# Performance work log

Hardware: AMD Instinct MI355X
Metric: run time of the kernel (lower is better)

The kernel has to match this reference:

```python
import jax, jax.numpy as jnp
import numpy as np
from jax import lax

HIDDEN = 64
EPS = 1e-6


def setup_inputs() -> dict:
    key = jax.random.key(0)
    ks = jax.random.split(key, 7)
    B, S, H = 2048, 2048, HIDDEN
    scale_ih = 1.0 / np.sqrt(2.0)
    scale_hh = 1.0 / np.sqrt(H)
    return {
        "residuals": jax.random.normal(ks[0], (B, S), dtype=jnp.float32),
        "W_ih_w": jax.random.uniform(ks[1], (H, 2), jnp.float32, -scale_ih, scale_ih),
        "W_ih_b": jax.random.uniform(ks[2], (H,), jnp.float32, -scale_ih, scale_ih),
        "W_hh_w": jax.random.uniform(ks[3], (H, H), jnp.float32, -scale_hh, scale_hh),
        "W_hh_b": jax.random.uniform(ks[4], (H,), jnp.float32, -scale_hh, scale_hh),
        "fc_w": jax.random.uniform(ks[5], (1, H), jnp.float32, -scale_hh, scale_hh),
        "fc_b": jax.random.uniform(ks[6], (1,), jnp.float32, -scale_hh, scale_hh),
    }


def reference(residuals, W_ih_w, W_ih_b, W_hh_w, W_hh_b, fc_w, fc_b):
    B, S = residuals.shape
    H = W_hh_w.shape[0]
    # torch.var is unbiased (ddof=1)
    sigma0 = jnp.var(residuals, axis=1, ddof=1)  # (B,)
    h0 = jnp.zeros((B, H), dtype=residuals.dtype)

    def step(carry, eps_prev):
        h, sigma = carry  # (B,H), (B,)
        inp = jnp.stack([eps_prev * eps_prev, sigma], axis=1)  # (B,2)
        h = inp @ W_ih_w.T + W_ih_b + h @ W_hh_w.T + W_hh_b  # (B,H)
        sigma = jax.nn.softplus(h @ fc_w.T + fc_b)[:, 0] + EPS  # (B,)
        return (h, sigma), sigma

    # eps at steps t=1..S-1 uses residuals[:, t-1]
    (_, _), sigmas = lax.scan(step, (h0, sigma0), residuals[:, :-1].T)  # (S-1, B)
    cond_vars = jnp.concatenate([sigma0[:, None], sigmas.T], axis=1)  # (B, S)
    return cond_vars
```

## Files before the change

kernel.cpp:

```cpp
#include <hip/hip_runtime.h>

#define S_LEN 2048

typedef float f32x4 __attribute__((ext_vector_type(4)));

__device__ __forceinline__ float rlane(float v, int l) {
    return __int_as_float(__builtin_amdgcn_readlane(__float_as_int(v), l));
}

template<int CTRL, int RM>
__device__ __forceinline__ float dpp_add(float v) {
    int t = __builtin_amdgcn_update_dpp(0, __float_as_int(v), CTRL, RM, 0xF, true);
    return v + __int_as_float(t);
}
__device__ __forceinline__ float wave_sum(float v) {
    v = dpp_add<0x111, 0xF>(v);
    v = dpp_add<0x112, 0xF>(v);
    v = dpp_add<0x114, 0xF>(v);
    v = dpp_add<0x118, 0xF>(v);
    v = dpp_add<0x142, 0xA>(v);
    v = dpp_add<0x143, 0xC>(v);
    return rlane(v, 63);
}
__device__ __forceinline__ float half_sum(float v, bool hf) {
    v = dpp_add<0x111, 0xF>(v);
    v = dpp_add<0x112, 0xF>(v);
    v = dpp_add<0x114, 0xF>(v);
    v = dpp_add<0x118, 0xF>(v);
    v = dpp_add<0x142, 0xA>(v);
    const float lo = rlane(v, 31);
    const float hi = rlane(v, 63);
    return hf ? hi : lo;
}

#if __has_builtin(__builtin_amdgcn_exp2f)
#define EXP2F(x) __builtin_amdgcn_exp2f(x)
#else
#define EXP2F(x) exp2f(x)
#endif
#if __has_builtin(__builtin_amdgcn_logf)
#define LOG2F(x) __builtin_amdgcn_logf(x)
#else
#define LOG2F(x) __log2f(x)
#endif

__attribute__((amdgpu_flat_work_group_size(512, 512)))
__attribute__((amdgpu_waves_per_eu(4, 8)))
__global__ void garch_fused(
    const float* __restrict__ res,
    const float* __restrict__ Wih,
    const float* __restrict__ bih,
    const float* __restrict__ Whh,
    const float* __restrict__ bhh,
    const float* __restrict__ fcw,
    const float* __restrict__ fcb,
    float* __restrict__ out)
{
    __shared__ __align__(16) float Wl[4096];
    __shared__ __align__(16) float tabA[1024];
    __shared__ __align__(16) float tabB[1024];
    __shared__ __align__(16) float ring[1024];
    __shared__ __align__(16) float ubuf[64];
    __shared__ float alpS[32], betS[32], gpreS[32], scS[4];

    const int tid  = threadIdx.x;
    const int lane = tid & 63;
    const int wv   = tid >> 6;
    const int l    = lane & 31;
    const bool hf  = (lane >= 32);

    const float Kc  = 1.44269504088896340736f;
    const float LN2 = 0.69314718055994530942f;

    {
        const f32x4* w4 = (const f32x4*)Whh;
        f32x4* wl4 = (f32x4*)Wl;
        for (int i = tid; i < 1024; i += 512) wl4[i] = w4[i];
    }
    __syncthreads();

    const int rp = blockIdx.x;
    const int p  = wv;
    const float* __restrict__ row  = res + (size_t)(2 * rp + (hf ? 1 : 0)) * S_LEN;
    float* __restrict__       orow = out + (size_t)(2 * rp + (hf ? 1 : 0)) * S_LEN;

    float* __restrict__ ringw = &ring[wv * 128 + (hf ? 64 : 0)];
    const int rotaddr = ((lane & 32) | ((l + 31) & 31)) << 2;

    float varh = 0.f, sigK = 0.f, carry = 0.f, ldn, eN_hold;
    int c0w, warm;

    if (p == 0) {
        float s1 = 0.f, s2 = 0.f;
#pragma unroll 8
        for (int i = 0; i < 64; ++i) {
            const float x = row[i * 32 + l];
            s1 += x;
            s2 = fmaf(x, x, s2);
        }
        s1 = half_sum(s1, hf);
        s2 = half_sum(s2, hf);
        const float mean = s1 * (1.0f / S_LEN);
        varh = (s2 - s1 * mean) * (1.0f / (S_LEN - 1));
        sigK = Kc * varh;
        carry = sigK;

        const float e0 = row[l], e1 = row[32 + l];
        ringw[l] = e0 * e0;
        ringw[32 + l] = 0.f;
        eN_hold = e1 * e1;
        ldn = row[64 + l];
        c0w = 0; warm = 0;
    } else {
        const int cw0 = 8 * p - 1;
        const float eP = row[(cw0 - 1) * 32 + l];
        const float eC = row[cw0 * 32 + l];
        const float eN = row[(cw0 + 1) * 32 + l];
        ringw[((cw0 - 1) & 1) * 32 + l] = eP * eP;
        ringw[(cw0 & 1) * 32 + l]       = eC * eC;
        eN_hold = eN * eN;
        ldn = row[(cw0 + 2) * 32 + l];
        c0w = cw0; warm = 1;
    }
    asm volatile("" ::: "memory");

    if (wv == 7) {
        const float w0l = Wih[lane * 2], w1l = Wih[lane * 2 + 1];
        const float blp = bih[lane] + bhh[lane];
        const float fl  = fcw[lane];

        const float A0  = Kc * wave_sum(fl * w0l);
        const float b0t = wave_sum(fl * w1l);
        const float Cg  = Kc * (wave_sum(fl * blp) + fcb[0]);
        if (lane == 0) { alpS[0] = A0; betS[0] = b0t; }
        float gpre_ = Cg, ginf_ = Cg;

        ubuf[lane] = fl;
        asm volatile("" ::: "memory");
        const f32x4* uq4 = (const f32x4*)ubuf;
        float u;
        {
            float n0 = 0.f, n1 = 0.f, n2 = 0.f, n3 = 0.f;
#pragma unroll 4
            for (int q = 0; q < 16; ++q) {
                const f32x4 uq = uq4[q];
                n0 = fmaf(Wl[(4 * q + 0) * 64 + lane], uq.x, n0);
                n1 = fmaf(Wl[(4 * q + 1) * 64 + lane], uq.y, n1);
                n2 = fmaf(Wl[(4 * q + 2) * 64 + lane], uq.z, n2);
                n3 = fmaf(Wl[(4 * q + 3) * 64 + lane], uq.w, n3);
            }
            u = (n0 + n1) + (n2 + n3);
        }
#pragma unroll 1
        for (int i = 1; i < 48; ++i) {
            const float daK = Kc * wave_sum(u * w0l);
            const float dbT = wave_sum(u * w1l);
            const float dgK = Kc * wave_sum(u * blp);
            if (lane == 0 && i < 32) { alpS[i] = daK; betS[i] = dbT; }
            gpre_ += (lane >= i) ? dgK : 0.f;
            ginf_ += dgK;
            ubuf[lane] = u;
            asm volatile("" ::: "memory");
            float n0 = 0.f, n1 = 0.f, n2 = 0.f, n3 = 0.f;
#pragma unroll 4
            for (int q = 0; q < 16; ++q) {
                const f32x4 uq = uq4[q];
                n0 = fmaf(Wl[(4 * q + 0) * 64 + lane], uq.x, n0);
                n1 = fmaf(Wl[(4 * q + 1) * 64 + lane], uq.y, n1);
                n2 = fmaf(Wl[(4 * q + 2) * 64 + lane], uq.z, n2);
                n3 = fmaf(Wl[(4 * q + 3) * 64 + lane], uq.w, n3);
            }
            u = (n0 + n1) + (n2 + n3);
        }
        asm volatile("" ::: "memory");
        for (int f = lane; f < 1024; f += 64) {
            const int lr = f >> 5, jc = f & 31;
            const int m = (lr - jc) & 31;
            const int dst = (((jc >> 2) * 32 + lr) << 2) + (jc & 3);
            tabA[dst] = (m < 4) ? 0.f : alpS[m];
            tabB[dst] = (m < 4) ? 0.f : betS[m];
        }
        if (lane < 32) gpreS[lane] = gpre_;
        if (lane == 0) scS[0] = ginf_;
    }
    __syncthreads();

    const float ginf = scS[0];
    const float bb0 = betS[0], bb1 = betS[1], bb2 = betS[2], bb3 = betS[3];
    const float Ka0 = alpS[0], Ka1 = alpS[1], Ka2 = alpS[2], Ka3 = alpS[3];

#define FIR4(DST, SB) { \
    const int a0_ = ((SB) << 5) + l; \
    const float x0_ = ringw[a0_]; \
    const float x1_ = ringw[(a0_ - 1) & 63]; \
    const float x2_ = ringw[(a0_ - 2) & 63]; \
    const float x3_ = ringw[(a0_ - 3) & 63]; \
    (DST) = fmaf(Ka3, x3_, fmaf(Ka2, x2_, fmaf(Ka1, x1_, Ka0 * x0_))); }

#define BCASTI(DST, V, IDX) { \
    const float lo_ = rlane((V), (IDX)); \
    const float hi_ = rlane((V), 32 + (IDX)); \
    (DST) = hf ? hi_ : lo_; }

    const f32x4* tA4 = (const f32x4*)tabA;
    const f32x4* tB4 = (const f32x4*)tabB;

    float acc, p1, p2, p3, vout = 0.f;

    if (p == 0) {
        float e4C;
        FIR4(e4C, 0);
        acc = gpreS[l] + e4C;
        BCASTI(p1, acc, 0); BCASTI(p2, acc, 1); BCASTI(p3, acc, 2);
        ringw[32 + l] = eN_hold;
        asm volatile("" ::: "memory");
    } else {
        const int cw0 = 8 * p - 1;
        float e4C;
        FIR4(e4C, cw0 & 1);
        acc = ginf + e4C;
        const f32x4* pq = (const f32x4*)(ringw + ((cw0 - 1) & 1) * 32);
#pragma unroll
        for (int q = 0; q < 8; ++q) {
            const f32x4 aqv = tA4[q * 32 + l];
            const f32x4 eq = pq[q];
#pragma unroll
            for (int w = 0; w < 4; ++w) {
                const int j = 4 * q + w;
                const float cf = (j > l) ? aqv[w] : 0.f;
                acc = fmaf(cf, eq[w], acc);
            }
        }
        BCASTI(p1, acc, 0); BCASTI(p2, acc, 1); BCASTI(p3, acc, 2);
        sigK = 0.f; carry = 0.f;
        ringw[((cw0 + 1) & 1) * 32 + l] = eN_hold;
        asm volatile("" ::: "memory");
    }

    const int ncc = 8 + warm;
    const bool p0 = (p == 0);

#pragma unroll 1
    for (int cc = 0; cc < ncc; ++cc) {
        const int c = c0w + cc;
        const int s = c & 1;
        float e4N;
        FIR4(e4N, s ^ 1);
        const float ginfE = ginf + e4N;
        const float sigchunk = carry;
        const f32x4* ringq = (const f32x4*)(ringw + (s << 5));

#pragma unroll
        for (int jg = 0; jg < 4; ++jg) {
            const f32x4 caq0 = tA4[(2 * jg) * 32 + l];
            const f32x4 caq1 = tA4[(2 * jg + 1) * 32 + l];
            const f32x4 cbq0 = tB4[(2 * jg) * 32 + l];
            const f32x4 cbq1 = tB4[(2 * jg + 1) * 32 + l];
            const f32x4 curA = ringq[jg * 2];
            const f32x4 curB = ringq[jg * 2 + 1];
#pragma unroll
            for (int k = 0; k < 8; ++k) {
                const int jj = (jg << 3) + k;
                const float ash = (k < 4) ? caq0[k] : caq1[k - 4];
                const float bsh = (k < 4) ? cbq0[k] : cbq1[k - 4];
                const float e2j = (k < 4) ? curA[k] : curB[k - 4];
                const float xp = fmaf(bb0, sigK, p1);
                acc = fmaf(bsh, sigK, acc);
                acc = fmaf(ash, e2j, acc);
                const bool mine = (l == jj);
                acc = mine ? ginfE : acc;
                const float tlo = rlane(acc, (jj + 3) & 31);
                const float thi = rlane(acc, 32 + ((jj + 3) & 31));
                const float t = hf ? thi : tlo;
                p1 = fmaf(bb1, sigK, p2);
                p2 = fmaf(bb2, sigK, p3);
                p3 = fmaf(bb3, sigK, t);
                const float ee = EXP2F(-__builtin_fabsf(xp));
                sigK = fmaxf(xp, 0.f) + LOG2F(1.0f + ee);
                vout = mine ? sigK : vout;
            }
        }

        if (cc >= warm) {
            const float rotv = __int_as_float(
                __builtin_amdgcn_ds_bpermute(rotaddr, __float_as_int(vout)));
            const float sv = (l == 0) ? sigchunk : rotv;
            float outv = fmaf(sv, LN2, 1e-6f);
            if (p0 && cc == 0) outv = (l == 0) ? varh : outv;
            orow[(c << 5) + l] = outv;
        }
        {
            const float c1v = rlane(vout, 31);
            const float c2v = rlane(vout, 63);
            carry = hf ? c2v : c1v;
        }
        ringw[(s << 5) + l] = ldn * ldn;
        const int nc3 = (c + 3 < 63) ? (c + 3) : 63;
        ldn = row[nc3 * 32 + l];
        asm volatile("" ::: "memory");
    }
#undef FIR4
#undef BCASTI
}

extern "C" void kernel_launch(void* const* d_in, const int* in_sizes, int n_in,
                              void* d_out, int out_size, void* d_ws, size_t ws_size,
                              hipStream_t stream) {
    const float* res = (const float*)d_in[0];
    const float* Wih = (const float*)d_in[1];
    const float* bih = (const float*)d_in[2];
    const float* Whh = (const float*)d_in[3];
    const float* bhh = (const float*)d_in[4];
    const float* fcw = (const float*)d_in[5];
    const float* fcb = (const float*)d_in[6];
    float* out = (float*)d_out;

    hipLaunchKernelGGL(garch_fused, dim3(1024), dim3(512), 0, stream,
                       res, Wih, bih, Whh, bhh, fcw, fcb, out);
}
```

Measured before the change: 213.7 us.

## Halve waves per row-pair and keep FIR coefficient tables in registers

Each block now uses 4 waves instead of 8, so each wave processes 16 chunks of 32 steps rather than 8. This halves the redundant warm-up and recompute work across the time-parallel waves. The per-lane alpha/beta coefficient tables move from LDS (tabA/tabB) into 64 VGPRs per lane, which removes LDS loads from the serial inner loop. The costs are a longer serial chain per wave and higher register pressure, which may reduce occupancy.

```diff
diff --git a/kernel.cpp b/kernel.cpp
--- a/kernel.cpp
+++ b/kernel.cpp
@@ -44,7 +44,7 @@
 #define LOG2F(x) __log2f(x)
 #endif
 
-__attribute__((amdgpu_flat_work_group_size(512, 512)))
+__attribute__((amdgpu_flat_work_group_size(256, 256)))
 __attribute__((amdgpu_waves_per_eu(4, 8)))
 __global__ void garch_fused(
     const float* __restrict__ res,
@@ -57,9 +57,7 @@
     float* __restrict__ out)
 {
     __shared__ __align__(16) float Wl[4096];
-    __shared__ __align__(16) float tabA[1024];
-    __shared__ __align__(16) float tabB[1024];
-    __shared__ __align__(16) float ring[1024];
+    __shared__ __align__(16) float ring[512];
     __shared__ __align__(16) float ubuf[64];
     __shared__ float alpS[32], betS[32], gpreS[32], scS[4];
 
@@ -75,7 +73,7 @@
     {
         const f32x4* w4 = (const f32x4*)Whh;
         f32x4* wl4 = (f32x4*)Wl;
-        for (int i = tid; i < 1024; i += 512) wl4[i] = w4[i];
+        for (int i = tid; i < 1024; i += 256) wl4[i] = w4[i];
     }
     __syncthreads();
 
@@ -112,7 +110,7 @@
         ldn = row[64 + l];
         c0w = 0; warm = 0;
     } else {
-        const int cw0 = 8 * p - 1;
+        const int cw0 = 16 * p - 1;
         const float eP = row[(cw0 - 1) * 32 + l];
         const float eC = row[cw0 * 32 + l];
         const float eN = row[(cw0 + 1) * 32 + l];
@@ -124,7 +122,7 @@
     }
     asm volatile("" ::: "memory");
 
-    if (wv == 7) {
+    if (wv == 3) {
         const float w0l = Wih[lane * 2], w1l = Wih[lane * 2 + 1];
         const float blp = bih[lane] + bhh[lane];
         const float fl  = fcw[lane];
@@ -173,13 +171,6 @@
             u = (n0 + n1) + (n2 + n3);
         }
         asm volatile("" ::: "memory");
-        for (int f = lane; f < 1024; f += 64) {
-            const int lr = f >> 5, jc = f & 31;
-            const int m = (lr - jc) & 31;
-            const int dst = (((jc >> 2) * 32 + lr) << 2) + (jc & 3);
-            tabA[dst] = (m < 4) ? 0.f : alpS[m];
-            tabB[dst] = (m < 4) ? 0.f : betS[m];
-        }
         if (lane < 32) gpreS[lane] = gpre_;
         if (lane == 0) scS[0] = ginf_;
     }
@@ -188,6 +179,22 @@
     const float ginf = scS[0];
     const float bb0 = betS[0], bb1 = betS[1], bb2 = betS[2], bb3 = betS[3];
     const float Ka0 = alpS[0], Ka1 = alpS[1], Ka2 = alpS[2], Ka3 = alpS[3];
+
+    f32x4 ca[8], cb[8];
+#pragma unroll
+    for (int q = 0; q < 8; ++q) {
+#pragma unroll
+        for (int w = 0; w < 4; ++w) {
+            const int m = (l - (4 * q + w)) & 31;
+            const bool z = (m < 4);
+            ca[q][w] = z ? 0.f : alpS[m];
+            cb[q][w] = z ? 0.f : betS[m];
+        }
+    }
+    asm("" : "+v"(ca[0]), "+v"(ca[1]), "+v"(ca[2]), "+v"(ca[3]),
+             "+v"(ca[4]), "+v"(ca[5]), "+v"(ca[6]), "+v"(ca[7]),
+             "+v"(cb[0]), "+v"(cb[1]), "+v"(cb[2]), "+v"(cb[3]),
+             "+v"(cb[4]), "+v"(cb[5]), "+v"(cb[6]), "+v"(cb[7]));
 
 #define FIR4(DST, SB) { \
     const int a0_ = ((SB) << 5) + l; \
@@ -202,9 +209,6 @@
     const float hi_ = rlane((V), 32 + (IDX)); \
     (DST) = hf ? hi_ : lo_; }
 
-    const f32x4* tA4 = (const f32x4*)tabA;
-    const f32x4* tB4 = (const f32x4*)tabB;
-
     float acc, p1, p2, p3, vout = 0.f;
 
     if (p == 0) {
@@ -215,19 +219,18 @@
         ringw[32 + l] = eN_hold;
         asm volatile("" ::: "memory");
     } else {
-        const int cw0 = 8 * p - 1;
+        const int cw0 = 16 * p - 1;
         float e4C;
         FIR4(e4C, cw0 & 1);
         acc = ginf + e4C;
         const f32x4* pq = (const f32x4*)(ringw + ((cw0 - 1) & 1) * 32);
 #pragma unroll
         for (int q = 0; q < 8; ++q) {
-            const f32x4 aqv = tA4[q * 32 + l];
             const f32x4 eq = pq[q];
 #pragma unroll
             for (int w = 0; w < 4; ++w) {
                 const int j = 4 * q + w;
-                const float cf = (j > l) ? aqv[w] : 0.f;
+                const float cf = (j > l) ? ca[q][w] : 0.f;
                 acc = fmaf(cf, eq[w], acc);
             }
         }
@@ -237,7 +240,7 @@
         asm volatile("" ::: "memory");
     }
 
-    const int ncc = 8 + warm;
+    const int ncc = 16 + warm;
     const bool p0 = (p == 0);
 
 #pragma unroll 1
@@ -252,17 +255,13 @@
 
 #pragma unroll
         for (int jg = 0; jg < 4; ++jg) {
-            const f32x4 caq0 = tA4[(2 * jg) * 32 + l];
-            const f32x4 caq1 = tA4[(2 * jg + 1) * 32 + l];
-            const f32x4 cbq0 = tB4[(2 * jg) * 32 + l];
-            const f32x4 cbq1 = tB4[(2 * jg + 1) * 32 + l];
             const f32x4 curA = ringq[jg * 2];
             const f32x4 curB = ringq[jg * 2 + 1];
 #pragma unroll
             for (int k = 0; k < 8; ++k) {
                 const int jj = (jg << 3) + k;
-                const float ash = (k < 4) ? caq0[k] : caq1[k - 4];
-                const float bsh = (k < 4) ? cbq0[k] : cbq1[k - 4];
+                const float ash = ca[jj >> 2][jj & 3];
+                const float bsh = cb[jj >> 2][jj & 3];
                 const float e2j = (k < 4) ? curA[k] : curB[k - 4];
                 const float xp = fmaf(bb0, sigK, p1);
                 acc = fmaf(bsh, sigK, acc);
@@ -315,6 +314,6 @@
     const float* fcb = (const float*)d_in[6];
     float* out = (float*)d_out;
 
-    hipLaunchKernelGGL(garch_fused, dim3(1024), dim3(512), 0, stream,
+    hipLaunchKernelGGL(garch_fused, dim3(1024), dim3(256), 0, stream,
                        res, Wih, bih, Whh, bhh, fcw, fcb, out);
 }
```

Result: faster. 189.6 us (-11.3%).

## Precompute eps-driven forcing per chunk before the serial sigma recurrence

Applied to the files above, without the earlier changes.

The eps-squared contribution (the 32-tap alpha FIR plus the constant term) is now computed up front for every chunk the wave will process and stored in shared memory, in place of the per-step alpha FMA and ring reads inside the serial loop. Beta coefficients are kept in registers (cb array) instead of the tabA/tabB shared tables, and scalar constants are read via readfirstlane. This shortens the critical dependency chain of the recurrence by removing one FMA and several LDS loads per step. In exchange it adds a serial prologue, extra register pressure, and reuses the W_hh shared buffer for the forcing values.

```diff
diff --git a/kernel.cpp b/kernel.cpp
--- a/kernel.cpp
+++ b/kernel.cpp
@@ -6,6 +6,9 @@
 
 __device__ __forceinline__ float rlane(float v, int l) {
     return __int_as_float(__builtin_amdgcn_readlane(__float_as_int(v), l));
+}
+__device__ __forceinline__ float rfl(float v) {
+    return __int_as_float(__builtin_amdgcn_readfirstlane(__float_as_int(v)));
 }
 
 template<int CTRL, int RM>
@@ -56,9 +59,7 @@
     const float* __restrict__ fcb,
     float* __restrict__ out)
 {
-    __shared__ __align__(16) float Wl[4096];
-    __shared__ __align__(16) float tabA[1024];
-    __shared__ __align__(16) float tabB[1024];
+    __shared__ __align__(16) float smem[5120];
     __shared__ __align__(16) float ring[1024];
     __shared__ __align__(16) float ubuf[64];
     __shared__ float alpS[32], betS[32], gpreS[32], scS[4];
@@ -74,7 +75,7 @@
 
     {
         const f32x4* w4 = (const f32x4*)Whh;
-        f32x4* wl4 = (f32x4*)Wl;
+        f32x4* wl4 = (f32x4*)smem;
         for (int i = tid; i < 1024; i += 512) wl4[i] = w4[i];
     }
     __syncthreads();
@@ -85,10 +86,11 @@
     float* __restrict__       orow = out + (size_t)(2 * rp + (hf ? 1 : 0)) * S_LEN;
 
     float* __restrict__ ringw = &ring[wv * 128 + (hf ? 64 : 0)];
+    float* __restrict__ Fw    = smem + wv * 640 + (hf ? 32 : 0);
     const int rotaddr = ((lane & 32) | ((l + 31) & 31)) << 2;
 
-    float varh = 0.f, sigK = 0.f, carry = 0.f, ldn, eN_hold;
-    int c0w, warm;
+    float varh = 0.f, sigK = 0.f, carry = 0.f, ldn;
+    int c0w, warm, nF;
 
     if (p == 0) {
         float s1 = 0.f, s2 = 0.f;
@@ -105,22 +107,19 @@
         sigK = Kc * varh;
         carry = sigK;
 
-        const float e0 = row[l], e1 = row[32 + l];
+        const float e0 = row[l];
+        ringw[32 + l] = 0.f;
         ringw[l] = e0 * e0;
-        ringw[32 + l] = 0.f;
-        eN_hold = e1 * e1;
-        ldn = row[64 + l];
-        c0w = 0; warm = 0;
+        ldn = row[32 + l];
+        c0w = 0; warm = 0; nF = 9;
     } else {
         const int cw0 = 8 * p - 1;
         const float eP = row[(cw0 - 1) * 32 + l];
         const float eC = row[cw0 * 32 + l];
-        const float eN = row[(cw0 + 1) * 32 + l];
         ringw[((cw0 - 1) & 1) * 32 + l] = eP * eP;
         ringw[(cw0 & 1) * 32 + l]       = eC * eC;
-        eN_hold = eN * eN;
-        ldn = row[(cw0 + 2) * 32 + l];
-        c0w = cw0; warm = 1;
+        ldn = row[(cw0 + 1) * 32 + l];
+        c0w = cw0; warm = 1; nF = 10;
     }
     asm volatile("" ::: "memory");
 
@@ -144,10 +143,10 @@
 #pragma unroll 4
             for (int q = 0; q < 16; ++q) {
                 const f32x4 uq = uq4[q];
-                n0 = fmaf(Wl[(4 * q + 0) * 64 + lane], uq.x, n0);
-                n1 = fmaf(Wl[(4 * q + 1) * 64 + lane], uq.y, n1);
-                n2 = fmaf(Wl[(4 * q + 2) * 64 + lane], uq.z, n2);
-                n3 = fmaf(Wl[(4 * q + 3) * 64 + lane], uq.w, n3);
+                n0 = fmaf(smem[(4 * q + 0) * 64 + lane], uq.x, n0);
+                n1 = fmaf(smem[(4 * q + 1) * 64 + lane], uq.y, n1);
+                n2 = fmaf(smem[(4 * q + 2) * 64 + lane], uq.z, n2);
+                n3 = fmaf(smem[(4 * q + 3) * 64 + lane], uq.w, n3);
             }
             u = (n0 + n1) + (n2 + n3);
         }
@@ -165,76 +164,64 @@
 #pragma unroll 4
             for (int q = 0; q < 16; ++q) {
                 const f32x4 uq = uq4[q];
-                n0 = fmaf(Wl[(4 * q + 0) * 64 + lane], uq.x, n0);
-                n1 = fmaf(Wl[(4 * q + 1) * 64 + lane], uq.y, n1);
-                n2 = fmaf(Wl[(4 * q + 2) * 64 + lane], uq.z, n2);
-                n3 = fmaf(Wl[(4 * q + 3) * 64 + lane], uq.w, n3);
+                n0 = fmaf(smem[(4 * q + 0) * 64 + lane], uq.x, n0);
+                n1 = fmaf(smem[(4 * q + 1) * 64 + lane], uq.y, n1);
+                n2 = fmaf(smem[(4 * q + 2) * 64 + lane], uq.z, n2);
+                n3 = fmaf(smem[(4 * q + 3) * 64 + lane], uq.w, n3);
             }
             u = (n0 + n1) + (n2 + n3);
         }
         asm volatile("" ::: "memory");
-        for (int f = lane; f < 1024; f += 64) {
-            const int lr = f >> 5, jc = f & 31;
-            const int m = (lr - jc) & 31;
-            const int dst = (((jc >> 2) * 32 + lr) << 2) + (jc & 3);
-            tabA[dst] = (m < 4) ? 0.f : alpS[m];
-            tabB[dst] = (m < 4) ? 0.f : betS[m];
-        }
         if (lane < 32) gpreS[lane] = gpre_;
         if (lane == 0) scS[0] = ginf_;
     }
     __syncthreads();
 
-    const float ginf = scS[0];
-    const float bb0 = betS[0], bb1 = betS[1], bb2 = betS[2], bb3 = betS[3];
-    const float Ka0 = alpS[0], Ka1 = alpS[1], Ka2 = alpS[2], Ka3 = alpS[3];
-
-#define FIR4(DST, SB) { \
-    const int a0_ = ((SB) << 5) + l; \
-    const float x0_ = ringw[a0_]; \
-    const float x1_ = ringw[(a0_ - 1) & 63]; \
-    const float x2_ = ringw[(a0_ - 2) & 63]; \
-    const float x3_ = ringw[(a0_ - 3) & 63]; \
-    (DST) = fmaf(Ka3, x3_, fmaf(Ka2, x2_, fmaf(Ka1, x1_, Ka0 * x0_))); }
-
-#define BCASTI(DST, V, IDX) { \
-    const float lo_ = rlane((V), (IDX)); \
-    const float hi_ = rlane((V), 32 + (IDX)); \
-    (DST) = hf ? hi_ : lo_; }
-
-    const f32x4* tA4 = (const f32x4*)tabA;
-    const f32x4* tB4 = (const f32x4*)tabB;
-
-    float acc, p1, p2, p3, vout = 0.f;
-
-    if (p == 0) {
-        float e4C;
-        FIR4(e4C, 0);
-        acc = gpreS[l] + e4C;
-        BCASTI(p1, acc, 0); BCASTI(p2, acc, 1); BCASTI(p3, acc, 2);
-        ringw[32 + l] = eN_hold;
-        asm volatile("" ::: "memory");
-    } else {
-        const int cw0 = 8 * p - 1;
-        float e4C;
-        FIR4(e4C, cw0 & 1);
-        acc = ginf + e4C;
-        const f32x4* pq = (const f32x4*)(ringw + ((cw0 - 1) & 1) * 32);
-#pragma unroll
-        for (int q = 0; q < 8; ++q) {
-            const f32x4 aqv = tA4[q * 32 + l];
-            const f32x4 eq = pq[q];
-#pragma unroll
-            for (int w = 0; w < 4; ++w) {
-                const int j = 4 * q + w;
-                const float cf = (j > l) ? aqv[w] : 0.f;
-                acc = fmaf(cf, eq[w], acc);
-            }
-        }
-        BCASTI(p1, acc, 0); BCASTI(p2, acc, 1); BCASTI(p3, acc, 2);
-        sigK = 0.f; carry = 0.f;
-        ringw[((cw0 + 1) & 1) * 32 + l] = eN_hold;
-        asm volatile("" ::: "memory");
+    const float ginf = rfl(scS[0]);
+    const float bb0 = rfl(betS[0]), bb1 = rfl(betS[1]);
+    const float bb2 = rfl(betS[2]), bb3 = rfl(betS[3]);
+
+    f32x4 cb[8];
+#pragma unroll
+    for (int q = 0; q < 8; ++q) {
+#pragma unroll
+        for (int w = 0; w < 4; ++w) {
+            const int m = (l - (4 * q + w)) & 31;
+            cb[q][w] = (m < 4) ? 0.f : betS[m];
+        }
+    }
+    asm("" : "+v"(cb[0]), "+v"(cb[1]), "+v"(cb[2]), "+v"(cb[3]),
+             "+v"(cb[4]), "+v"(cb[5]), "+v"(cb[6]), "+v"(cb[7]));
+
+    {
+        const volatile float* aV = alpS;
+        int gc = c0w;
+#pragma unroll 1
+        for (int ci = 0; ci < nF; ++ci, ++gc) {
+            const int s = gc & 1;
+            const int a0 = (s << 5) + l;
+            float Fv = (p == 0 && ci == 0) ? gpreS[l] : ginf;
+#pragma unroll
+            for (int m = 0; m < 32; ++m)
+                Fv = fmaf(aV[m], ringw[(a0 - m) & 63], Fv);
+            Fw[ci * 64 + l] = Fv;
+            asm volatile("" ::: "memory");
+            ringw[((s ^ 1) << 5) + l] = ldn * ldn;
+            const int nc = (gc + 2 < 64) ? (gc + 2) : 63;
+            ldn = row[nc * 32 + l];
+            asm volatile("" ::: "memory");
+        }
+    }
+
+    float acc = Fw[l];
+    float p1, p2, p3, vout = 0.f;
+    {
+        const float lo0 = rlane(acc, 0), hi0 = rlane(acc, 32);
+        const float lo1 = rlane(acc, 1), hi1 = rlane(acc, 33);
+        const float lo2 = rlane(acc, 2), hi2 = rlane(acc, 34);
+        p1 = hf ? hi0 : lo0;
+        p2 = hf ? hi1 : lo1;
+        p3 = hf ? hi2 : lo2;
     }
 
     const int ncc = 8 + warm;
@@ -243,32 +230,22 @@
 #pragma unroll 1
     for (int cc = 0; cc < ncc; ++cc) {
         const int c = c0w + cc;
-        const int s = c & 1;
-        float e4N;
-        FIR4(e4N, s ^ 1);
-        const float ginfE = ginf + e4N;
         const float sigchunk = carry;
-        const f32x4* ringq = (const f32x4*)(ringw + (s << 5));
+        const float* Fn = Fw + (cc + 1) * 64;
 
 #pragma unroll
         for (int jg = 0; jg < 4; ++jg) {
-            const f32x4 caq0 = tA4[(2 * jg) * 32 + l];
-            const f32x4 caq1 = tA4[(2 * jg + 1) * 32 + l];
-            const f32x4 cbq0 = tB4[(2 * jg) * 32 + l];
-            const f32x4 cbq1 = tB4[(2 * jg + 1) * 32 + l];
-            const f32x4 curA = ringq[jg * 2];
-            const f32x4 curB = ringq[jg * 2 + 1];
+            const f32x4 Fq0 = *(const f32x4*)(Fn + jg * 8);
+            const f32x4 Fq1 = *(const f32x4*)(Fn + jg * 8 + 4);
 #pragma unroll
             for (int k = 0; k < 8; ++k) {
                 const int jj = (jg << 3) + k;
-                const float ash = (k < 4) ? caq0[k] : caq1[k - 4];
-                const float bsh = (k < 4) ? cbq0[k] : cbq1[k - 4];
-                const float e2j = (k < 4) ? curA[k] : curB[k - 4];
+                const float bsh = cb[jj >> 2][jj & 3];
+                const float Fv = (k < 4) ? Fq0[k] : Fq1[k - 4];
                 const float xp = fmaf(bb0, sigK, p1);
                 acc = fmaf(bsh, sigK, acc);
-                acc = fmaf(ash, e2j, acc);
                 const bool mine = (l == jj);
-                acc = mine ? ginfE : acc;
+                acc = mine ? Fv : acc;
                 const float tlo = rlane(acc, (jj + 3) & 31);
                 const float thi = rlane(acc, 32 + ((jj + 3) & 31));
                 const float t = hf ? thi : tlo;
@@ -294,13 +271,7 @@
             const float c2v = rlane(vout, 63);
             carry = hf ? c2v : c1v;
         }
-        ringw[(s << 5) + l] = ldn * ldn;
-        const int nc3 = (c + 3 < 63) ? (c + 3) : 63;
-        ldn = row[nc3 * 32 + l];
-        asm volatile("" ::: "memory");
-    }
-#undef FIR4
-#undef BCASTI
+    }
 }
 
 extern "C" void kernel_launch(void* const* d_in, const int* in_sizes, int n_in,
```

Result: slower. 231.5 us (+8.3%).
